# Kernel optimization log

Hardware: AMD Instinct MI355X
Metric: run time of the kernel (lower is better)

Reference implementation:

```python
import jax, jax.numpy as jnp
import numpy as np

EPS = 1e-5
GROUPS = 16
OUT_CH = 128
GC = OUT_CH // GROUPS  # group_channels = 8
SPAN = 128


def _bn(x, gamma, beta, axes):
    # BatchNorm in training mode: biased batch statistics over `axes`.
    m = jnp.mean(x, axis=axes, keepdims=True)
    v = jnp.var(x, axis=axes, keepdims=True)
    shape = [1] * x.ndim
    shape[1] = x.shape[1]
    g = gamma.reshape(shape)
    b = beta.reshape(shape)
    return (x - m) * jax.lax.rsqrt(v + EPS) * g + b


def setup_inputs() -> dict:
    key = jax.random.key(0)
    ks = jax.random.split(key, 3)
    x = jax.random.normal(ks[0], (2, 128, 64, 128), dtype=jnp.float32)
    W_qkv = jax.random.normal(ks[1], (2 * OUT_CH, 128), dtype=jnp.float32) * (1.0 / np.sqrt(128))
    rel_emb = jax.random.normal(ks[2], (2 * GC, 2 * SPAN - 1), dtype=jnp.float32)
    return {
        "x": x,
        "W_qkv": W_qkv,
        "gamma_qkv": jnp.ones((2 * OUT_CH,), jnp.float32),
        "beta_qkv": jnp.zeros((2 * OUT_CH,), jnp.float32),
        "rel_emb": rel_emb,
        "gamma_sim": jnp.ones((3 * GROUPS,), jnp.float32),
        "beta_sim": jnp.zeros((3 * GROUPS,), jnp.float32),
        "gamma_out": jnp.ones((2 * OUT_CH,), jnp.float32),
        "beta_out": jnp.zeros((2 * OUT_CH,), jnp.float32),
    }


def reference(x, W_qkv, gamma_qkv, beta_qkv, rel_emb, gamma_sim, beta_sim, gamma_out, beta_out):
    # dim == 1: attend over the width axis. x: [B, C, H, W], W == SPAN.
    B, C, H, W = x.shape
    xr = jnp.transpose(x, (0, 2, 1, 3)).reshape(B * H, C, W)  # [BH, C, W]

    # 1x1 Conv1d + BN1d -> query/key/value
    qkv = jnp.einsum('oc,bcl->bol', W_qkv, xr)  # [BH, 2*OUT, W]
    qkv = _bn(qkv, gamma_qkv, beta_qkv, axes=(0, 2))
    qkv = qkv.reshape(B * H, GROUPS, 2 * GC, W)
    q = qkv[:, :, : GC // 2]            # [BH, g, gc/2, W]
    k = qkv[:, :, GC // 2: GC]          # [BH, g, gc/2, W]
    v = qkv[:, :, GC:]                  # [BH, g, gc,   W]

    # relative position embeddings gathered into [2*gc, span, span]
    idx = jnp.arange(SPAN)[:, None] - jnp.arange(SPAN)[None, :] + SPAN - 1
    emb = rel_emb[:, idx]               # [2*gc, span, span]
    q_emb = emb[: GC // 2]
    k_emb = emb[GC // 2: GC]
    v_emb = emb[GC:]

    qe = jnp.einsum('bgci,cij->bgij', q, q_emb)   # [BH, g, W, W]
    ke = jnp.einsum('bgci,cij->bgij', k, k_emb)   # [BH, g, W, W]
    # faithful to original: contracts the first spatial axis of qe/ke
    qk = jnp.einsum('bgci,bgcj->bgij', qe, ke)    # [BH, g, W, W]

    sim = jnp.concatenate([qk, qe, ke], axis=1)   # [BH, 3g, W, W]
    sim = _bn(sim, gamma_sim, beta_sim, axes=(0, 2, 3))
    sim = sim.reshape(B * H, 3, GROUPS, W, W).sum(axis=1)  # [BH, g, W, W]
    sim = jax.nn.softmax(sim, axis=3)

    am = jnp.einsum('bgij,bgcj->bgci', sim, v)      # [BH, g, gc, W]
    ame = jnp.einsum('bgij,cij->bgci', sim, v_emb)  # [BH, g, gc, W]

    out = jnp.concatenate([am, ame], axis=-1).reshape(B * H, 2 * OUT_CH, W)
    out = _bn(out, gamma_out, beta_out, axes=(0, 2))
    out = out.reshape(B, H, OUT_CH, 2, W).sum(axis=-2)  # [B, H, OUT, W]
    return jnp.transpose(out, (0, 2, 1, 3))             # [B, OUT, H, W]
```

## Files before the change

### kernel.cpp

```cpp
#include <hip/hip_runtime.h>

#define EPS 1e-5f
typedef unsigned short u16;
typedef unsigned int u32;

typedef __attribute__((ext_vector_type(8))) short bf16x8;
typedef __attribute__((ext_vector_type(4))) float f32x4;

__device__ __forceinline__ float bf2f(u16 h) {
    u32 u = ((u32)h) << 16;
    return __builtin_bit_cast(float, u);
}
__device__ __forceinline__ u16 f2bf(float f) {
    u32 u = __builtin_bit_cast(u32, f);
    u32 r = (u + 0x7fffu + ((u >> 16) & 1u)) >> 16;
    return (u16)r;
}
__device__ __forceinline__ u32 pack2(float a, float b) {
    return (u32)f2bf(a) | ((u32)f2bf(b) << 16);
}
__device__ __forceinline__ float bflo(u32 u) {
    return __builtin_bit_cast(float, u << 16);
}
__device__ __forceinline__ float bfhi(u32 u) {
    return __builtin_bit_cast(float, u & 0xffff0000u);
}

__global__ __launch_bounds__(256) void k1_gemm_qkv(
    const float* __restrict__ x, const float* __restrict__ Wq,
    float* __restrict__ qkv, float* __restrict__ stats)
{
    __shared__ float Wt[64 * 68];
    __shared__ float xt[64 * 128];
    const int tid = threadIdx.x;
    const int ot = blockIdx.x;
    const int n  = blockIdx.y;
    const int b = n >> 6, h = n & 63;
    const int to = tid >> 5, tl = tid & 31;
    const int o0 = to * 8, l0 = tl * 4;

    float acc[8][4];
#pragma unroll
    for (int r = 0; r < 8; ++r) { acc[r][0]=0.f; acc[r][1]=0.f; acc[r][2]=0.f; acc[r][3]=0.f; }

    for (int cb = 0; cb < 128; cb += 64) {
        __syncthreads();
#pragma unroll
        for (int k = 0; k < 4; ++k) {
            int f = tid + k * 256;
            int oo = f >> 4, c4 = f & 15;
            float4 v = *(const float4*)(Wq + (ot * 64 + oo) * 128 + cb + c4 * 4);
            *(float4*)(Wt + oo * 68 + c4 * 4) = v;
        }
#pragma unroll
        for (int k = 0; k < 8; ++k) {
            int f = tid + k * 256;
            int c = f >> 5, l4 = f & 31;
            float4 v = *(const float4*)(x + ((size_t)((b * 128 + cb + c) * 64 + h)) * 128 + l4 * 4);
            *(float4*)(xt + c * 128 + l4 * 4) = v;
        }
        __syncthreads();
#pragma unroll 4
        for (int c = 0; c < 64; ++c) {
            float4 xv = *(const float4*)(xt + c * 128 + l0);
#pragma unroll
            for (int r = 0; r < 8; ++r) {
                float w = Wt[(o0 + r) * 68 + c];
                acc[r][0] += w * xv.x; acc[r][1] += w * xv.y;
                acc[r][2] += w * xv.z; acc[r][3] += w * xv.w;
            }
        }
    }

#pragma unroll
    for (int r = 0; r < 8; ++r) {
        int o = ot * 64 + o0 + r;
        *(float4*)(qkv + ((size_t)n * 256 + o) * 128 + l0) =
            make_float4(acc[r][0], acc[r][1], acc[r][2], acc[r][3]);
        float s  = acc[r][0] + acc[r][1] + acc[r][2] + acc[r][3];
        float sq = acc[r][0]*acc[r][0] + acc[r][1]*acc[r][1] + acc[r][2]*acc[r][2] + acc[r][3]*acc[r][3];
#pragma unroll
        for (int m = 1; m < 32; m <<= 1) {
            s  += __shfl_xor(s, m);
            sq += __shfl_xor(sq, m);
        }
        if (tl == 0) {
            atomicAdd(&stats[o], s);
            atomicAdd(&stats[256 + o], sq);
        }
    }
}

__global__ void k3_coef_qkv(const float* __restrict__ stats,
                            const float* __restrict__ gamma, const float* __restrict__ beta,
                            float* __restrict__ coef)
{
    int o = threadIdx.x;
    const float cnt = 16384.f;
    float mean = stats[o] / cnt;
    float var  = stats[256 + o] / cnt - mean * mean;
    float a = gamma[o] * rsqrtf(var + EPS);
    coef[o] = a;
    coef[256 + o] = beta[o] - a * mean;
}

__global__ __launch_bounds__(512, 4) void k4_pass1(
    const float* __restrict__ qkv, const float* __restrict__ rel,
    const float* __restrict__ cq, u16* __restrict__ qk,
    float* __restrict__ stats)
{
    __shared__ u16 QEb[128 * 136];
    __shared__ u16 KEb[128 * 136];
    __shared__ float red[8 * 6];
    const int tid = threadIdx.x;
    const int n = blockIdx.x >> 4, g = blockIdx.x & 15;

    const int pt = tid & 31, pi = tid >> 5;
    const int t0 = pt * 4, i0 = pi * 8;
    const int d0 = t0 - i0 + 120;

    float qes = 0.f, qesq = 0.f, kes = 0.f, kesq = 0.f;

#pragma unroll
    for (int mat = 0; mat < 2; ++mat) {
        float qv[4][4];
#pragma unroll
        for (int c = 0; c < 4; ++c) {
            int o = g * 16 + mat * 4 + c;
            float a = cq[o], bb = cq[256 + o];
            float4 x0 = *(const float4*)(qkv + ((size_t)n * 256 + o) * 128 + t0);
            qv[c][0] = fmaf(a, x0.x, bb); qv[c][1] = fmaf(a, x0.y, bb);
            qv[c][2] = fmaf(a, x0.z, bb); qv[c][3] = fmaf(a, x0.w, bb);
        }
        float rr[4][12];
#pragma unroll
        for (int c = 0; c < 4; ++c) {
            const float* p = rel + (mat * 4 + c) * 255 + d0;
#pragma unroll
            for (int j = 0; j < 3; ++j) {
                float4 v = *(const float4*)(p + j * 4);
                rr[c][j*4+0] = v.x; rr[c][j*4+1] = v.y;
                rr[c][j*4+2] = v.z; rr[c][j*4+3] = v.w;
            }
        }
        u16* MB = mat ? KEb : QEb;
        float s = 0.f, sq = 0.f;
#pragma unroll
        for (int ii = 0; ii < 8; ++ii) {
            float vv[4];
#pragma unroll
            for (int tt = 0; tt < 4; ++tt) {
                int dl = tt - ii + 7;
                float v = qv[0][tt] * rr[0][dl] + qv[1][tt] * rr[1][dl]
                        + qv[2][tt] * rr[2][dl] + qv[3][tt] * rr[3][dl];
                vv[tt] = v;
                s += v; sq = fmaf(v, v, sq);
            }
            *(uint2*)(MB + (i0 + ii) * 136 + t0) =
                make_uint2(pack2(vv[0], vv[1]), pack2(vv[2], vv[3]));
        }
        if (mat == 0) { qes = s; qesq = sq; } else { kes = s; kesq = sq; }
    }
    __syncthreads();

    const int lane = tid & 63, wv = tid >> 6;
    const int fm = lane & 15, fq = lane >> 4;

    f32x4 acc[8];
#pragma unroll
    for (int tj = 0; tj < 8; ++tj) acc[tj] = (f32x4){0.f, 0.f, 0.f, 0.f};

#pragma unroll
    for (int kb = 0; kb < 4; ++kb) {
        const int ko = kb * 32 + fq * 8;
        bf16x8 a0 = *(const bf16x8*)(QEb + (wv * 16 + fm) * 136 + ko);
#pragma unroll
        for (int tj = 0; tj < 8; ++tj) {
            bf16x8 bfr = *(const bf16x8*)(KEb + (tj * 16 + fm) * 136 + ko);
            acc[tj] = __builtin_amdgcn_mfma_f32_16x16x32_bf16(a0, bfr, acc[tj], 0, 0, 0);
        }
    }

    float qks = 0.f, qksq = 0.f;
#pragma unroll
    for (int tj = 0; tj < 8; ++tj) {
#pragma unroll
        for (int r = 0; r < 4; ++r) {
            float v = acc[tj][r];
            qks += v; qksq = fmaf(v, v, qksq);
            QEb[(wv * 16 + fq * 4 + r) * 136 + tj * 16 + fm] = f2bf(v);
        }
    }

#pragma unroll
    for (int m = 1; m < 64; m <<= 1) {
        qes += __shfl_xor(qes, m);  qesq += __shfl_xor(qesq, m);
        kes += __shfl_xor(kes, m);  kesq += __shfl_xor(kesq, m);
        qks += __shfl_xor(qks, m);  qksq += __shfl_xor(qksq, m);
    }
    if (lane == 0) {
        red[wv * 6 + 0] = qes; red[wv * 6 + 1] = qesq;
        red[wv * 6 + 2] = kes; red[wv * 6 + 3] = kesq;
        red[wv * 6 + 4] = qks; red[wv * 6 + 5] = qksq;
    }
    __syncthreads();

    u16* qkg = qk + (size_t)(n * 16 + g) * 16384;
#pragma unroll
    for (int k = 0; k < 4; ++k) {
        int f = tid + k * 512;
        int row = f >> 4, c8 = f & 15;
        uint4 v = *(const uint4*)(QEb + row * 136 + c8 * 8);
        *(uint4*)(qkg + ((c8 >> 1) * 128 + row) * 16 + (c8 & 1) * 8) = v;
    }

    if (tid < 6) {
        float tot = 0.f;
#pragma unroll
        for (int w = 0; w < 8; ++w) tot += red[w * 6 + tid];
        int off = (tid & 1) ? 560 : 512;
        int ch = (tid < 2) ? (16 + g) : (tid < 4) ? (32 + g) : g;
        atomicAdd(&stats[off + ch], tot);
    }
}

__global__ void k5_coef_sim(const float* __restrict__ stats,
                            const float* __restrict__ gamma, const float* __restrict__ beta,
                            float* __restrict__ coef)
{
    int ch = threadIdx.x;
    if (ch < 48) {
        const float cnt = 2097152.f;
        float mean = stats[512 + ch] / cnt;
        float var  = stats[560 + ch] / cnt - mean * mean;
        float a = gamma[ch] * rsqrtf(var + EPS);
        coef[ch] = a;
        coef[48 + ch] = beta[ch] - a * mean;
    }
}

#define K6_ST1(rb, rv, vv, qkf)                                              \
    {                                                                        \
        float qe = q0 * bf2f((u16)rb[0]) + q1 * bf2f((u16)rb[1])             \
                 + q2 * bf2f((u16)rb[2]) + q3 * bf2f((u16)rb[3]);            \
        float ke = k0 * bf2f((u16)rb[4]) + k1 * bf2f((u16)rb[5])             \
                 + k2 * bf2f((u16)rb[6]) + k3 * bf2f((u16)rb[7]);            \
        float s = fmaf(aqk, (qkf), qe + ke);                                 \
        float e = __expf(s);                                                 \
        l += e;                                                              \
        _Pragma("unroll")                                                    \
        for (int c = 0; c < 8; ++c) {                                        \
            am[c]  = fmaf(e, bf2f((u16)vv[c]), am[c]);                       \
            ame[c] = fmaf(e, bf2f((u16)rv[c]), ame[c]);                      \
        }                                                                    \
    }

#define K6_LOADU(S, u)                                                       \
    {                                                                        \
        const u16* rp_ = relb + (i + 126 - 2 * (u)) * 24;                    \
        S##rb1 = *(const bf16x8*)(rp_);                                      \
        S##rv1 = *(const bf16x8*)(rp_ + 8);                                  \
        S##rb0 = *(const bf16x8*)(rp_ + 24);                                 \
        S##rv0 = *(const bf16x8*)(rp_ + 32);                                 \
        S##vv0 = *(const bf16x8*)(vb + (u) * 16);                            \
        S##vv1 = *(const bf16x8*)(vb + (u) * 16 + 8);                        \
    }

#define K6_UNIT(CS, NS, u, wrd)                                              \
    {                                                                        \
        if ((u) < 63) { K6_LOADU(NS, (u) + 1); }                             \
        __builtin_amdgcn_sched_barrier(0);                                   \
        K6_ST1(CS##rb0, CS##rv0, CS##vv0, bflo(wrd));                        \
        K6_ST1(CS##rb1, CS##rv1, CS##vv1, bfhi(wrd));                        \
    }

__global__ __launch_bounds__(128, 4) void k6_pass2(
    const float* __restrict__ qkv, const float* __restrict__ rel,
    const float* __restrict__ cq, const float* __restrict__ cs,
    const u16* __restrict__ qk,
    float* __restrict__ outraw, float* __restrict__ ostats)
{
    __shared__ u16 relb[256 * 24];
    __shared__ u16 vb[128 * 8];
    __shared__ float qn_s[8 * 128];
    const int tid = threadIdx.x;
    const int n = blockIdx.x >> 4, g = blockIdx.x & 15;

#pragma unroll
    for (int k = 0; k < 32; ++k) {
        int f = tid + k * 128;
        int c = f >> 8, d = f & 255;
        if (d < 255) relb[d * 24 + c] = f2bf(rel[c * 255 + d]);
    }
#pragma unroll
    for (int k = 0; k < 8; ++k) {
        int f = tid + k * 128;
        int c = f >> 7, t = f & 127;
        int o = g * 16 + c;
        qn_s[f] = fmaf(cq[o], qkv[((size_t)n * 256 + o) * 128 + t], cq[256 + o]);
    }
#pragma unroll
    for (int k = 0; k < 8; ++k) {
        int f = tid + k * 128;
        int c = f >> 7, j = f & 127;
        int o = g * 16 + 8 + c;
        float v = fmaf(cq[o], qkv[((size_t)n * 256 + o) * 128 + j], cq[256 + o]);
        vb[j * 8 + c] = f2bf(v);
    }
    __syncthreads();

    const float aqk = cs[g], aqe = cs[16 + g], ake = cs[32 + g];
    const int i = tid;

    bf16x8 Arb0, Arb1, Arv0, Arv1, Avv0, Avv1;
    bf16x8 Brb0, Brb1, Brv0, Brv1, Bvv0, Bvv1;

    const u16* qkg = qk + (size_t)(n * 16 + g) * 16384 + i * 16;

    uint4 qA = *(const uint4*)(qkg);
    uint4 qB = *(const uint4*)(qkg + 8);
    K6_LOADU(A, 0);

    float q0 = aqe * qn_s[i],       q1 = aqe * qn_s[128 + i];
    float q2 = aqe * qn_s[256 + i], q3 = aqe * qn_s[384 + i];
    float k0 = ake * qn_s[512 + i], k1 = ake * qn_s[640 + i];
    float k2 = ake * qn_s[768 + i], k3 = ake * qn_s[896 + i];

    float l = 0.f;
    float am[8], ame[8];
#pragma unroll
    for (int c = 0; c < 8; ++c) { am[c] = 0.f; ame[c] = 0.f; }

#pragma unroll
    for (int jc = 0; jc < 8; ++jc) {
        uint4 nA, nB;
        if (jc < 7) {
            nA = *(const uint4*)(qkg + (jc + 1) * 2048);
            nB = *(const uint4*)(qkg + (jc + 1) * 2048 + 8);
        }

        K6_UNIT(A, B, jc * 8 + 0, qA.x);
        K6_UNIT(B, A, jc * 8 + 1, qA.y);
        K6_UNIT(A, B, jc * 8 + 2, qA.z);
        K6_UNIT(B, A, jc * 8 + 3, qA.w);
        K6_UNIT(A, B, jc * 8 + 4, qB.x);
        K6_UNIT(B, A, jc * 8 + 5, qB.y);
        K6_UNIT(A, B, jc * 8 + 6, qB.z);
        K6_UNIT(B, A, jc * 8 + 7, qB.w);

        if (jc < 7) { qA = nA; qB = nB; }
    }

    float inv = 1.f / l;
    float o16[16];
#pragma unroll
    for (int c = 0; c < 8; ++c) { o16[2 * c] = am[c] * inv; o16[2 * c + 1] = ame[c] * inv; }

    float* orow = outraw + ((size_t)n * 256 + g * 16) * 128 + i;
#pragma unroll
    for (int c16 = 0; c16 < 16; ++c16) orow[c16 * 128] = o16[c16];

    const int lane = tid & 63;
#pragma unroll
    for (int c16 = 0; c16 < 16; ++c16) {
        float sv = o16[c16], sq = o16[c16] * o16[c16];
#pragma unroll
        for (int mm = 1; mm < 64; mm <<= 1) { sv += __shfl_xor(sv, mm); sq += __shfl_xor(sq, mm); }
        if (lane == 0) {
            atomicAdd(&ostats[g * 16 + c16], sv);
            atomicAdd(&ostats[256 + g * 16 + c16], sq);
        }
    }
}

__global__ void k7_coef_out(const float* __restrict__ stats,
                            const float* __restrict__ gamma, const float* __restrict__ beta,
                            float* __restrict__ coef)
{
    int o = threadIdx.x;
    const float cnt = 16384.f;
    float mean = stats[608 + o] / cnt;
    float var  = stats[864 + o] / cnt - mean * mean;
    float a = gamma[o] * rsqrtf(var + EPS);
    coef[o] = a;
    coef[256 + o] = beta[o] - a * mean;
}

__global__ __launch_bounds__(256) void k8_final(
    const float* __restrict__ outraw, const float* __restrict__ co,
    float* __restrict__ out)
{
    int idx = blockIdx.x * 256 + threadIdx.x;
    int w  = idx & 127;
    int h  = (idx >> 7) & 63;
    int oc = (idx >> 13) & 127;
    int b  = idx >> 20;
    int n  = b * 64 + h;
    int o0 = oc * 2;
    float x0 = outraw[((size_t)n * 256 + o0) * 128 + w];
    float x1 = outraw[((size_t)n * 256 + o0 + 1) * 128 + w];
    out[idx] = (co[o0] * x0 + co[256 + o0]) + (co[o0 + 1] * x1 + co[256 + o0 + 1]);
}

extern "C" void kernel_launch(void* const* d_in, const int* in_sizes, int n_in,
                              void* d_out, int out_size, void* d_ws, size_t ws_size,
                              hipStream_t stream)
{
    const float* x   = (const float*)d_in[0];
    const float* Wq  = (const float*)d_in[1];
    const float* gq  = (const float*)d_in[2];
    const float* bq  = (const float*)d_in[3];
    const float* rel = (const float*)d_in[4];
    const float* gs  = (const float*)d_in[5];
    const float* bs  = (const float*)d_in[6];
    const float* go  = (const float*)d_in[7];
    const float* bo  = (const float*)d_in[8];

    float* ws     = (float*)d_ws;
    float* qkv    = ws;
    float* outraw = ws + 4194304;
    u16*   qk     = (u16*)(ws + 8388608);
    float* stats  = ws + 25165824;
    float* cq     = stats + 1120;
    float* cs     = stats + 1632;
    float* co     = stats + 1728;

    (void)hipMemsetAsync(stats, 0, 1120 * sizeof(float), stream);

    k1_gemm_qkv<<<dim3(4, 128), 256, 0, stream>>>(x, Wq, qkv, stats);
    k3_coef_qkv<<<1, 256, 0, stream>>>(stats, gq, bq, cq);
    k4_pass1<<<2048, 512, 0, stream>>>(qkv, rel, cq, qk, stats);
    k5_coef_sim<<<1, 64, 0, stream>>>(stats, gs, bs, cs);
    k6_pass2<<<2048, 128, 0, stream>>>(qkv, rel, cq, cs, qk, outraw, stats + 608);
    k7_coef_out<<<1, 256, 0, stream>>>(stats, go, bo, co);
    k8_final<<<8192, 256, 0, stream>>>(outraw, co, (float*)d_out);
}
```

Measured before the change: 355.2 us.

## Split pass2 key range across two thread halves and keep values fp32 in LDS

The pass-2 attention kernel now runs 256 threads per block. Each half of the block handles half of the 128 key positions for the same query row, and the two partial accumulators are combined through shared memory at the end. The v and v-embedding operands are stored in LDS as fp32 instead of bf16, which removes the per-element conversions in the inner loop. The explicit double-buffered prefetch and sched barriers are gone, and loads are grouped four keys at a time. In exchange the kernel uses more LDS, adds an extra barrier and reduction, and leaves half the threads idle during the final write-out and stats step.

```diff
diff --git a/kernel.cpp b/kernel.cpp
--- a/kernel.cpp
+++ b/kernel.cpp
@@ -239,136 +239,152 @@
     }
 }
 
-#define K6_ST1(rb, rv, vv, qkf)                                              \
+#define K6_S(rb, rva, rvb, vva, vvb, qkf)                                    \
     {                                                                        \
         float qe = q0 * bf2f((u16)rb[0]) + q1 * bf2f((u16)rb[1])             \
                  + q2 * bf2f((u16)rb[2]) + q3 * bf2f((u16)rb[3]);            \
         float ke = k0 * bf2f((u16)rb[4]) + k1 * bf2f((u16)rb[5])             \
                  + k2 * bf2f((u16)rb[6]) + k3 * bf2f((u16)rb[7]);            \
-        float s = fmaf(aqk, (qkf), qe + ke);                                 \
-        float e = __expf(s);                                                 \
+        float e = __expf(fmaf(aqk, (qkf), qe + ke));                         \
         l += e;                                                              \
-        _Pragma("unroll")                                                    \
-        for (int c = 0; c < 8; ++c) {                                        \
-            am[c]  = fmaf(e, bf2f((u16)vv[c]), am[c]);                       \
-            ame[c] = fmaf(e, bf2f((u16)rv[c]), ame[c]);                      \
-        }                                                                    \
-    }
-
-#define K6_LOADU(S, u)                                                       \
+        am[0] = fmaf(e, vva.x, am[0]); am[1] = fmaf(e, vva.y, am[1]);        \
+        am[2] = fmaf(e, vva.z, am[2]); am[3] = fmaf(e, vva.w, am[3]);        \
+        am[4] = fmaf(e, vvb.x, am[4]); am[5] = fmaf(e, vvb.y, am[5]);        \
+        am[6] = fmaf(e, vvb.z, am[6]); am[7] = fmaf(e, vvb.w, am[7]);        \
+        ame[0] = fmaf(e, rva.x, ame[0]); ame[1] = fmaf(e, rva.y, ame[1]);    \
+        ame[2] = fmaf(e, rva.z, ame[2]); ame[3] = fmaf(e, rva.w, ame[3]);    \
+        ame[4] = fmaf(e, rvb.x, ame[4]); ame[5] = fmaf(e, rvb.y, ame[5]);    \
+        ame[6] = fmaf(e, rvb.z, ame[6]); ame[7] = fmaf(e, rvb.w, ame[7]);    \
+    }
+
+#define K6_G4(jb, w0, w1)                                                    \
     {                                                                        \
-        const u16* rp_ = relb + (i + 126 - 2 * (u)) * 24;                    \
-        S##rb1 = *(const bf16x8*)(rp_);                                      \
-        S##rv1 = *(const bf16x8*)(rp_ + 8);                                  \
-        S##rb0 = *(const bf16x8*)(rp_ + 24);                                 \
-        S##rv0 = *(const bf16x8*)(rp_ + 32);                                 \
-        S##vv0 = *(const bf16x8*)(vb + (u) * 16);                            \
-        S##vv1 = *(const bf16x8*)(vb + (u) * 16 + 8);                        \
-    }
-
-#define K6_UNIT(CS, NS, u, wrd)                                              \
-    {                                                                        \
-        if ((u) < 63) { K6_LOADU(NS, (u) + 1); }                             \
-        __builtin_amdgcn_sched_barrier(0);                                   \
-        K6_ST1(CS##rb0, CS##rv0, CS##vv0, bflo(wrd));                        \
-        K6_ST1(CS##rb1, CS##rv1, CS##vv1, bfhi(wrd));                        \
-    }
-
-__global__ __launch_bounds__(128, 4) void k6_pass2(
+        const char* rp = smem + (D - (jb)) * 48;                             \
+        bf16x8 rb0 = *(const bf16x8*)(rp);                                   \
+        bf16x8 rb1 = *(const bf16x8*)(rp - 48);                              \
+        bf16x8 rb2 = *(const bf16x8*)(rp - 96);                              \
+        bf16x8 rb3 = *(const bf16x8*)(rp - 144);                             \
+        float4 rv0a = *(const float4*)(rp + 16);                             \
+        float4 rv0b = *(const float4*)(rp + 32);                             \
+        float4 rv1a = *(const float4*)(rp - 32);                             \
+        float4 rv1b = *(const float4*)(rp - 16);                             \
+        float4 rv2a = *(const float4*)(rp - 80);                             \
+        float4 rv2b = *(const float4*)(rp - 64);                             \
+        float4 rv3a = *(const float4*)(rp - 128);                            \
+        float4 rv3b = *(const float4*)(rp - 112);                            \
+        const float* vp = vbf + (jb) * 8;                                    \
+        float4 vv0a = *(const float4*)(vp);                                  \
+        float4 vv0b = *(const float4*)(vp + 4);                              \
+        float4 vv1a = *(const float4*)(vp + 8);                              \
+        float4 vv1b = *(const float4*)(vp + 12);                             \
+        float4 vv2a = *(const float4*)(vp + 16);                             \
+        float4 vv2b = *(const float4*)(vp + 20);                             \
+        float4 vv3a = *(const float4*)(vp + 24);                             \
+        float4 vv3b = *(const float4*)(vp + 28);                             \
+        K6_S(rb0, rv0a, rv0b, vv0a, vv0b, bflo(w0));                         \
+        K6_S(rb1, rv1a, rv1b, vv1a, vv1b, bfhi(w0));                         \
+        K6_S(rb2, rv2a, rv2b, vv2a, vv2b, bflo(w1));                         \
+        K6_S(rb3, rv3a, rv3b, vv3a, vv3b, bfhi(w1));                         \
+    }
+
+__global__ __launch_bounds__(256, 4) void k6_pass2(
     const float* __restrict__ qkv, const float* __restrict__ rel,
     const float* __restrict__ cq, const float* __restrict__ cs,
     const u16* __restrict__ qk,
     float* __restrict__ outraw, float* __restrict__ ostats)
 {
-    __shared__ u16 relb[256 * 24];
-    __shared__ u16 vb[128 * 8];
-    __shared__ float qn_s[8 * 128];
+    __shared__ __align__(64) char smem[20480];
+    float* vbf  = (float*)(smem + 12288);
+    float* qn_s = (float*)(smem + 16384);
     const int tid = threadIdx.x;
     const int n = blockIdx.x >> 4, g = blockIdx.x & 15;
 
 #pragma unroll
-    for (int k = 0; k < 32; ++k) {
-        int f = tid + k * 128;
-        int c = f >> 8, d = f & 255;
-        if (d < 255) relb[d * 24 + c] = f2bf(rel[c * 255 + d]);
-    }
-#pragma unroll
-    for (int k = 0; k < 8; ++k) {
-        int f = tid + k * 128;
+    for (int c = 0; c < 16; ++c) {
+        if (tid < 255) {
+            float v = rel[c * 255 + tid];
+            if (c < 8) *(u16*)(smem + tid * 48 + c * 2) = f2bf(v);
+            else       *(float*)(smem + tid * 48 + 16 + (c - 8) * 4) = v;
+        }
+    }
+#pragma unroll
+    for (int k = 0; k < 4; ++k) {
+        int f = tid + k * 256;
         int c = f >> 7, t = f & 127;
         int o = g * 16 + c;
         qn_s[f] = fmaf(cq[o], qkv[((size_t)n * 256 + o) * 128 + t], cq[256 + o]);
     }
 #pragma unroll
-    for (int k = 0; k < 8; ++k) {
-        int f = tid + k * 128;
+    for (int k = 0; k < 4; ++k) {
+        int f = tid + k * 256;
         int c = f >> 7, j = f & 127;
         int o = g * 16 + 8 + c;
-        float v = fmaf(cq[o], qkv[((size_t)n * 256 + o) * 128 + j], cq[256 + o]);
-        vb[j * 8 + c] = f2bf(v);
+        vbf[j * 8 + c] = fmaf(cq[o], qkv[((size_t)n * 256 + o) * 128 + j], cq[256 + o]);
     }
     __syncthreads();
 
     const float aqk = cs[g], aqe = cs[16 + g], ake = cs[32 + g];
-    const int i = tid;
-
-    bf16x8 Arb0, Arb1, Arv0, Arv1, Avv0, Avv1;
-    bf16x8 Brb0, Brb1, Brv0, Brv1, Bvv0, Bvv1;
-
-    const u16* qkg = qk + (size_t)(n * 16 + g) * 16384 + i * 16;
-
-    uint4 qA = *(const uint4*)(qkg);
-    uint4 qB = *(const uint4*)(qkg + 8);
-    K6_LOADU(A, 0);
+    const int i = tid & 127, hf = tid >> 7;
+    const int D = i + 127;
 
     float q0 = aqe * qn_s[i],       q1 = aqe * qn_s[128 + i];
     float q2 = aqe * qn_s[256 + i], q3 = aqe * qn_s[384 + i];
     float k0 = ake * qn_s[512 + i], k1 = ake * qn_s[640 + i];
     float k2 = ake * qn_s[768 + i], k3 = ake * qn_s[896 + i];
 
+    const u16* qkg = qk + (size_t)(n * 16 + g) * 16384 + i * 16;
+
     float l = 0.f;
     float am[8], ame[8];
 #pragma unroll
     for (int c = 0; c < 8; ++c) { am[c] = 0.f; ame[c] = 0.f; }
 
 #pragma unroll
-    for (int jc = 0; jc < 8; ++jc) {
-        uint4 nA, nB;
-        if (jc < 7) {
-            nA = *(const uint4*)(qkg + (jc + 1) * 2048);
-            nB = *(const uint4*)(qkg + (jc + 1) * 2048 + 8);
-        }
-
-        K6_UNIT(A, B, jc * 8 + 0, qA.x);
-        K6_UNIT(B, A, jc * 8 + 1, qA.y);
-        K6_UNIT(A, B, jc * 8 + 2, qA.z);
-        K6_UNIT(B, A, jc * 8 + 3, qA.w);
-        K6_UNIT(A, B, jc * 8 + 4, qB.x);
-        K6_UNIT(B, A, jc * 8 + 5, qB.y);
-        K6_UNIT(A, B, jc * 8 + 6, qB.z);
-        K6_UNIT(B, A, jc * 8 + 7, qB.w);
-
-        if (jc < 7) { qA = nA; qB = nB; }
-    }
-
-    float inv = 1.f / l;
-    float o16[16];
-#pragma unroll
-    for (int c = 0; c < 8; ++c) { o16[2 * c] = am[c] * inv; o16[2 * c + 1] = ame[c] * inv; }
-
-    float* orow = outraw + ((size_t)n * 256 + g * 16) * 128 + i;
-#pragma unroll
-    for (int c16 = 0; c16 < 16; ++c16) orow[c16 * 128] = o16[c16];
-
-    const int lane = tid & 63;
-#pragma unroll
-    for (int c16 = 0; c16 < 16; ++c16) {
-        float sv = o16[c16], sq = o16[c16] * o16[c16];
-#pragma unroll
-        for (int mm = 1; mm < 64; mm <<= 1) { sv += __shfl_xor(sv, mm); sq += __shfl_xor(sq, mm); }
-        if (lane == 0) {
-            atomicAdd(&ostats[g * 16 + c16], sv);
-            atomicAdd(&ostats[256 + g * 16 + c16], sq);
+    for (int jq = 0; jq < 4; ++jq) {
+        const int jc = hf * 4 + jq;
+        const uint4 qA = *(const uint4*)(qkg + jc * 2048);
+        const uint4 qB = *(const uint4*)(qkg + jc * 2048 + 8);
+        const int jb = jc * 16;
+        K6_G4(jb,      qA.x, qA.y);
+        K6_G4(jb + 4,  qA.z, qA.w);
+        K6_G4(jb + 8,  qB.x, qB.y);
+        K6_G4(jb + 12, qB.z, qB.w);
+    }
+
+    __syncthreads();
+    float* red = (float*)smem;
+    if (hf) {
+        float* r = red + i * 17;
+#pragma unroll
+        for (int c = 0; c < 8; ++c) { r[c] = am[c]; r[8 + c] = ame[c]; }
+        r[16] = l;
+    }
+    __syncthreads();
+    if (!hf) {
+        const float* r = red + i * 17;
+#pragma unroll
+        for (int c = 0; c < 8; ++c) { am[c] += r[c]; ame[c] += r[8 + c]; }
+        l += r[16];
+
+        float inv = 1.f / l;
+        float o16[16];
+#pragma unroll
+        for (int c = 0; c < 8; ++c) { o16[2 * c] = am[c] * inv; o16[2 * c + 1] = ame[c] * inv; }
+
+        float* orow = outraw + ((size_t)n * 256 + g * 16) * 128 + i;
+#pragma unroll
+        for (int c16 = 0; c16 < 16; ++c16) orow[c16 * 128] = o16[c16];
+
+        const int lane = tid & 63;
+#pragma unroll
+        for (int c16 = 0; c16 < 16; ++c16) {
+            float sv = o16[c16], sq = o16[c16] * o16[c16];
+#pragma unroll
+            for (int mm = 1; mm < 64; mm <<= 1) { sv += __shfl_xor(sv, mm); sq += __shfl_xor(sq, mm); }
+            if (lane == 0) {
+                atomicAdd(&ostats[g * 16 + c16], sv);
+                atomicAdd(&ostats[256 + g * 16 + c16], sq);
+            }
         }
     }
 }
@@ -431,7 +447,7 @@
     k3_coef_qkv<<<1, 256, 0, stream>>>(stats, gq, bq, cq);
     k4_pass1<<<2048, 512, 0, stream>>>(qkv, rel, cq, qk, stats);
     k5_coef_sim<<<1, 64, 0, stream>>>(stats, gs, bs, cs);
-    k6_pass2<<<2048, 128, 0, stream>>>(qkv, rel, cq, cs, qk, outraw, stats + 608);
+    k6_pass2<<<2048, 256, 0, stream>>>(qkv, rel, cq, cs, qk, outraw, stats + 608);
     k7_coef_out<<<1, 256, 0, stream>>>(stats, go, bo, co);
     k8_final<<<8192, 256, 0, stream>>>(outraw, co, (float*)d_out);
 }
```

Measured after the change: 407.6 us. 14.7% more time.
